# Kernel optimization log

Hardware: AMD Instinct MI355X
Metric: run time of the kernel (lower is better)

## Reference

```python
import jax, jax.numpy as jnp
import numpy as np
import math

B, SQ, SKV, H = 8, 1024, 1024, 1024
NH, HD = 16, 64  # num_attention_heads, attention_head_size


def setup_inputs() -> dict:
    key = jax.random.key(0)
    ks = jax.random.split(key, 6)
    s = 1.0 / math.sqrt(H)
    return {
        "hidden_states": jax.random.normal(ks[0], (B, SQ, H), jnp.float32),
        "keyvalue_states": jax.random.normal(ks[1], (B, SKV, H), jnp.float32),
        "attention_mask": jnp.zeros((B, 1, 1, SKV), jnp.float32),
        "Wq": jax.random.normal(ks[2], (H, H), jnp.float32) * s,
        "bq": jnp.zeros((H,), jnp.float32),
        "Wk": jax.random.normal(ks[3], (H, H), jnp.float32) * s,
        "bk": jnp.zeros((H,), jnp.float32),
        "Wv": jax.random.normal(ks[4], (H, H), jnp.float32) * s,
        "bv": jnp.zeros((H,), jnp.float32),
    }


def _split_heads(x):
    # [B, S, H] -> [B, NH, S, HD]
    b, s, _ = x.shape
    return x.reshape(b, s, NH, HD).transpose(0, 2, 1, 3)


def reference(hidden_states, keyvalue_states, attention_mask, Wq, bq, Wk, bk, Wv, bv):
    q = _split_heads(hidden_states @ Wq.T + bq)     # [B, NH, SQ, HD]
    k = _split_heads(keyvalue_states @ Wk.T + bk)   # [B, NH, SKV, HD]
    v = _split_heads(keyvalue_states @ Wv.T + bv)   # [B, NH, SKV, HD]
    scores = jnp.einsum("bhqd,bhkd->bhqk", q, k) / math.sqrt(HD)
    scores = scores + attention_mask                 # additive mask broadcast
    probs = jax.nn.softmax(scores, axis=-1)          # dropout = identity (eval)
    ctx = jnp.einsum("bhqk,bhkd->bhqd", probs, v)
    ctx = ctx.transpose(0, 2, 1, 3).reshape(hidden_states.shape[0], -1, NH * HD)
    return ctx
```

## Files before the change

### kernel.cpp

```cpp
#include <hip/hip_runtime.h>
#include <hip/hip_bf16.h>


typedef __attribute__((ext_vector_type(8))) short short8;
typedef __attribute__((ext_vector_type(4))) short short4v;
typedef __attribute__((ext_vector_type(4))) float f32x4;
typedef __attribute__((ext_vector_type(2))) float f32x2;
typedef __attribute__((ext_vector_type(16))) float f32x16;
typedef __attribute__((ext_vector_type(2))) unsigned uint2v;
typedef __attribute__((ext_vector_type(4))) int int4v;

#define AS1(p) ((const __attribute__((address_space(1))) void*)(p))
#define AS3(p) ((__attribute__((address_space(3))) void*)(p))

__device__ inline short f2bs(float x) {
    __hip_bfloat16 h = __float2bfloat16(x);
    return *reinterpret_cast<short*>(&h);
}

__global__ __launch_bounds__(256) void cvt_bf16(
    const float* __restrict__ s0, const float* __restrict__ s1,
    const float* __restrict__ s2, const float* __restrict__ s3,
    const float* __restrict__ s4,
    short* __restrict__ d0, short* __restrict__ d1,
    short* __restrict__ d2, short* __restrict__ d3, short* __restrict__ d4)
{
    const float* s; short* d; int n4;
    switch (blockIdx.y) {
        case 0: s = s0; d = d0; n4 = 2097152; break;
        case 1: s = s1; d = d1; n4 = 2097152; break;
        case 2: s = s2; d = d2; n4 = 262144;  break;
        case 3: s = s3; d = d3; n4 = 262144;  break;
        default: s = s4; d = d4; n4 = 262144; break;
    }
    for (int i = blockIdx.x * 256 + threadIdx.x; i < n4; i += gridDim.x * 256) {
        float4 v = ((const float4*)s)[i];
        short4v o;
        o.x = f2bs(v.x); o.y = f2bs(v.y); o.z = f2bs(v.z); o.w = f2bs(v.w);
        ((short4v*)d)[i] = o;
    }
}

__global__ __launch_bounds__(256, 2) void q_gemm(
    const short* __restrict__ hsb, const short* __restrict__ wqb,
    const float* __restrict__ bq, short* __restrict__ qo)
{
    __shared__ __align__(16) short As[128 * 64];
    __shared__ __align__(16) short Bs[128 * 64];

    const int t = threadIdx.x;
    const int lane = t & 63;
    const int wave = t >> 6;
    const int lane31 = lane & 31;
    const int hi = lane >> 5;
    const int wm = (wave & 1) * 64;
    const int wn = (wave >> 1) * 64;
    const int m0 = blockIdx.x * 128;
    const int n0 = blockIdx.y * 128;

    f32x16 acc[2][2] = {};

    for (int k0 = 0; k0 < 1024; k0 += 64) {
        #pragma unroll
        for (int i = 0; i < 4; ++i) {
            int c = i * 256 + t;
            int row = c >> 3;
            int gc = (c & 7) ^ (row & 7);
            __builtin_amdgcn_global_load_lds(
                AS1(&hsb[(size_t)(m0 + row) * 1024 + k0 + gc * 8]), AS3(&As[c * 8]), 16, 0, 0);
            __builtin_amdgcn_global_load_lds(
                AS1(&wqb[(size_t)(n0 + row) * 1024 + k0 + gc * 8]), AS3(&Bs[c * 8]), 16, 0, 0);
        }
        __syncthreads();

        #pragma unroll
        for (int kc = 0; kc < 4; ++kc) {
            short8 af[2], bf[2];
            #pragma unroll
            for (int mt = 0; mt < 2; ++mt) {
                int rr = wm + mt * 32 + lane31;
                af[mt] = *(short8*)&As[rr * 64 + ((kc * 2 + hi) ^ (rr & 7)) * 8];
            }
            #pragma unroll
            for (int nt = 0; nt < 2; ++nt) {
                int rn = wn + nt * 32 + lane31;
                bf[nt] = *(short8*)&Bs[rn * 64 + ((kc * 2 + hi) ^ (rn & 7)) * 8];
            }
            #pragma unroll
            for (int mt = 0; mt < 2; ++mt)
                #pragma unroll
                for (int nt = 0; nt < 2; ++nt)
                    acc[mt][nt] = __builtin_amdgcn_mfma_f32_32x32x16_bf16(
                        af[mt], bf[nt], acc[mt][nt], 0, 0, 0);
        }
        __syncthreads();
    }

    #pragma unroll
    for (int nt = 0; nt < 2; ++nt) {
        int col = n0 + wn + nt * 32 + lane31;
        float bb = bq[col];
        int h = col >> 6, d = col & 63;
        #pragma unroll
        for (int mt = 0; mt < 2; ++mt) {
            #pragma unroll
            for (int rg = 0; rg < 4; ++rg) {
                int m = m0 + wm + mt * 32 + rg * 8 + hi * 4;
                int b = m >> 10, s = m & 1023;
                size_t base = (size_t)((b * 16 + h) * 1024 + s) * 64 + d;
                #pragma unroll
                for (int r = 0; r < 4; ++r)
                    qo[base + (size_t)r * 64] = f2bs(acc[mt][nt][rg * 4 + r] + bb);
            }
        }
    }
}

__global__ __launch_bounds__(256, 2) void kv_gemm(
    const short* __restrict__ kvb,
    const short* __restrict__ wkb, const short* __restrict__ wvb,
    const float* __restrict__ bk, const float* __restrict__ bv,
    short* __restrict__ ko, short* __restrict__ vo)
{
    __shared__ __align__(16) short As[128 * 64];
    __shared__ __align__(16) short Bk[128 * 64];
    __shared__ __align__(16) short Bv[128 * 64];

    const int t = threadIdx.x;
    const int lane = t & 63;
    const int wave = t >> 6;
    const int lane31 = lane & 31;
    const int hi = lane >> 5;
    const int wm = (wave & 1) * 64;
    const int wn = (wave >> 1) * 64;
    const int m0 = blockIdx.x * 128;
    const int n0 = blockIdx.y * 128;

    f32x16 acck[2][2] = {};
    f32x16 accv[2][2] = {};

    for (int k0 = 0; k0 < 1024; k0 += 64) {
        #pragma unroll
        for (int i = 0; i < 4; ++i) {
            int c = i * 256 + t;
            int row = c >> 3;
            int gc = (c & 7) ^ (row & 7);
            __builtin_amdgcn_global_load_lds(
                AS1(&kvb[(size_t)(m0 + row) * 1024 + k0 + gc * 8]), AS3(&As[c * 8]), 16, 0, 0);
            __builtin_amdgcn_global_load_lds(
                AS1(&wkb[(size_t)(n0 + row) * 1024 + k0 + gc * 8]), AS3(&Bk[c * 8]), 16, 0, 0);
            __builtin_amdgcn_global_load_lds(
                AS1(&wvb[(size_t)(n0 + row) * 1024 + k0 + gc * 8]), AS3(&Bv[c * 8]), 16, 0, 0);
        }
        __syncthreads();

        #pragma unroll
        for (int kc = 0; kc < 4; ++kc) {
            short8 af[2], bfk[2], bfv[2];
            #pragma unroll
            for (int mt = 0; mt < 2; ++mt) {
                int rr = wm + mt * 32 + lane31;
                af[mt] = *(short8*)&As[rr * 64 + ((kc * 2 + hi) ^ (rr & 7)) * 8];
            }
            #pragma unroll
            for (int nt = 0; nt < 2; ++nt) {
                int rn = wn + nt * 32 + lane31;
                int off = rn * 64 + ((kc * 2 + hi) ^ (rn & 7)) * 8;
                bfk[nt] = *(short8*)&Bk[off];
                bfv[nt] = *(short8*)&Bv[off];
            }
            #pragma unroll
            for (int mt = 0; mt < 2; ++mt)
                #pragma unroll
                for (int nt = 0; nt < 2; ++nt) {
                    acck[mt][nt] = __builtin_amdgcn_mfma_f32_32x32x16_bf16(
                        af[mt], bfk[nt], acck[mt][nt], 0, 0, 0);
                    accv[mt][nt] = __builtin_amdgcn_mfma_f32_32x32x16_bf16(
                        af[mt], bfv[nt], accv[mt][nt], 0, 0, 0);
                }
        }
        __syncthreads();
    }

    #pragma unroll
    for (int nt = 0; nt < 2; ++nt) {
        int col = n0 + wn + nt * 32 + lane31;
        float bb = bk[col];
        int h = col >> 6, d = col & 63;
        #pragma unroll
        for (int mt = 0; mt < 2; ++mt) {
            #pragma unroll
            for (int rg = 0; rg < 4; ++rg) {
                int m = m0 + wm + mt * 32 + rg * 8 + hi * 4;
                int b = m >> 10, s = m & 1023;
                size_t base = (size_t)((b * 16 + h) * 1024 + s) * 64 + d;
                #pragma unroll
                for (int r = 0; r < 4; ++r)
                    ko[base + (size_t)r * 64] = f2bs(acck[mt][nt][rg * 4 + r] + bb);
            }
        }
    }
    #pragma unroll
    for (int nt = 0; nt < 2; ++nt) {
        int col = n0 + wn + nt * 32 + lane31;
        float bb = bv[col];
        int h = col >> 6, d = col & 63;
        #pragma unroll
        for (int mt = 0; mt < 2; ++mt) {
            #pragma unroll
            for (int rg = 0; rg < 4; ++rg) {
                int m = m0 + wm + mt * 32 + rg * 8 + hi * 4;
                int b = m >> 10, s = m & 1023;
                short4v pk;
                pk.x = f2bs(accv[mt][nt][rg * 4 + 0] + bb);
                pk.y = f2bs(accv[mt][nt][rg * 4 + 1] + bb);
                pk.z = f2bs(accv[mt][nt][rg * 4 + 2] + bb);
                pk.w = f2bs(accv[mt][nt][rg * 4 + 3] + bb);
                *(short4v*)&vo[(size_t)((b * 16 + h) * 64 + d) * 1024 + s] = pk;
            }
        }
    }
}

#define EXPC 0.18033688011112042f
#define LOG2E 1.4426950408889634f

__device__ inline uint2v half_swap(unsigned c, unsigned d, int hi) {
#if __has_builtin(__builtin_amdgcn_permlane32_swap)
    return __builtin_amdgcn_permlane32_swap(c, d, false, false);
#else
    unsigned send = hi ? c : d;
    unsigned recv = (unsigned)__shfl_xor((int)send, 32, 64);
    uint2v r;
    r.x = hi ? recv : c;
    r.y = hi ? d : recv;
    return r;
#endif
}

__device__ inline float fast_exp2(float x) {
#if __has_builtin(__builtin_amdgcn_exp2f)
    return __builtin_amdgcn_exp2f(x);
#else
    float r;
    asm("v_exp_f32 %0, %1" : "=v"(r) : "v"(x));
    return r;
#endif
}

__device__ inline unsigned cvt_pk_bf16(float a, float b) {
    unsigned r;
    asm("v_cvt_pk_bf16_f32 %0, %1, %2" : "=v"(r) : "v"(a), "v"(b));
    return r;
}

__global__ __launch_bounds__(256, 4) void attn(
    const short* __restrict__ q, const short* __restrict__ k,
    const short* __restrict__ vt, const float* __restrict__ mask,
    float* __restrict__ out)
{
    __shared__ __align__(16) short Ks[2][64 * 64];
    __shared__ __align__(16) short Vs[2][64 * 64];
    __shared__ __align__(16) float Ems[1024];

    const int t = threadIdx.x;
    const int lane = t & 63;
    const int wq = t >> 6;
    const int lane31 = lane & 31;
    const int hi = lane >> 5;

    const int id = blockIdx.x;
    const int bh = (id >> 6) * 8 + (id & 7);
    const int qt = (id >> 3) & 7;
    const int b = bh >> 4, h = bh & 15;

    const short* qbase = q + (size_t)(bh * 1024 + qt * 128) * 64;
    const short* kbase = k + (size_t)bh * 1024 * 64;
    const short* vbase = vt + (size_t)bh * 64 * 1024;

    {
        float4 mv = ((const float4*)(mask + b * 1024))[t];
        float4 o4;
        o4.x = mv.x * LOG2E; o4.y = mv.y * LOG2E;
        o4.z = mv.z * LOG2E; o4.w = mv.w * LOG2E;
        *(float4*)&Ems[t * 4] = o4;
    }

    short8 qf[4];
    #pragma unroll
    for (int kc = 0; kc < 4; ++kc)
        qf[kc] = *(const short8*)&qbase[(size_t)(wq * 32 + lane31) * 64 + kc * 16 + hi * 8];

    #pragma unroll
    for (int i = 0; i < 2; ++i) {
        int c = i * 256 + t;
        int row = c >> 3;
        int gc = (c & 7) ^ (row & 7);
        __builtin_amdgcn_global_load_lds(AS1(kbase + (size_t)row * 64 + gc * 8),
                                         AS3(&Ks[0][c * 8]), 16, 0, 0);
        __builtin_amdgcn_global_load_lds(AS1(vbase + (size_t)row * 1024 + gc * 8),
                                         AS3(&Vs[0][c * 8]), 16, 0, 0);
    }

    f32x16 o_acc[2] = {};
    f32x2 lacc = {0.f, 0.f};

    for (int kt = 0; kt < 16; ++kt) {
        __syncthreads();
        if (kt < 15) {
            int kv1 = (kt + 1) * 64;
            int nb = (kt + 1) & 1;
            #pragma unroll
            for (int i = 0; i < 2; ++i) {
                int c = i * 256 + t;
                int row = c >> 3;
                int gc = (c & 7) ^ (row & 7);
                __builtin_amdgcn_global_load_lds(
                    AS1(kbase + (size_t)(kv1 + row) * 64 + gc * 8),
                    AS3(&Ks[nb][c * 8]), 16, 0, 0);
                __builtin_amdgcn_global_load_lds(
                    AS1(vbase + (size_t)row * 1024 + kv1 + gc * 8),
                    AS3(&Vs[nb][c * 8]), 16, 0, 0);
            }
        }
        const short* ks_ = Ks[kt & 1];
        const short* vs_ = Vs[kt & 1];
        const int kv0 = kt * 64;

        f32x16 sacc[2] = {};
        #pragma unroll
        for (int kc = 0; kc < 4; ++kc) {
            #pragma unroll
            for (int mt = 0; mt < 2; ++mt) {
                int rr = mt * 32 + lane31;
                short8 ak = *(short8*)&ks_[rr * 64 + ((kc * 2 + hi) ^ (rr & 7)) * 8];
                sacc[mt] = __builtin_amdgcn_mfma_f32_32x32x16_bf16(ak, qf[kc], sacc[mt], 0, 0, 0);
            }
        }

        unsigned pk[2][4][2];
        #pragma unroll
        for (int mt = 0; mt < 2; ++mt) {
            #pragma unroll
            for (int rg = 0; rg < 4; ++rg) {
                int kvl = mt * 32 + rg * 8 + hi * 4;
                f32x4 mk = *(const f32x4*)&Ems[kv0 + kvl];
                f32x4 sv;
                sv.x = sacc[mt][rg * 4 + 0];
                sv.y = sacc[mt][rg * 4 + 1];
                sv.z = sacc[mt][rg * 4 + 2];
                sv.w = sacc[mt][rg * 4 + 3];
                f32x4 ev = sv * EXPC + mk;
                float p0 = fast_exp2(ev.x);
                float p1 = fast_exp2(ev.y);
                float p2 = fast_exp2(ev.z);
                float p3 = fast_exp2(ev.w);
                f32x2 pa; pa.x = p0; pa.y = p2;
                f32x2 pb; pb.x = p1; pb.y = p3;
                lacc += pa + pb;
                pk[mt][rg][0] = cvt_pk_bf16(p0, p1);
                pk[mt][rg][1] = cvt_pk_bf16(p2, p3);
            }
        }

        #pragma unroll
        for (int kc = 0; kc < 4; ++kc) {
            const int mt = kc >> 1, glo = (kc & 1) * 2;
            uint2v s0 = half_swap(pk[mt][glo][0], pk[mt][glo + 1][0], hi);
            uint2v s1 = half_swap(pk[mt][glo][1], pk[mt][glo + 1][1], hi);
            int4v fr; fr.x = (int)s0.x; fr.y = (int)s1.x; fr.z = (int)s0.y; fr.w = (int)s1.y;
            short8 ap = *(short8*)&fr;
            #pragma unroll
            for (int nt = 0; nt < 2; ++nt) {
                int rv = nt * 32 + lane31;
                short8 bv_ = *(short8*)&vs_[rv * 64 + ((kc * 2 + hi) ^ (rv & 7)) * 8];
                o_acc[nt] = __builtin_amdgcn_mfma_f32_32x32x16_bf16(ap, bv_, o_acc[nt], 0, 0, 0);
            }
        }
    }

    float l_sum = lacc.x + lacc.y;
    l_sum += __shfl_xor(l_sum, 32, 64);
    float invl = 1.f / l_sum;

    #pragma unroll
    for (int rg = 0; rg < 4; ++rg) {
        #pragma unroll
        for (int r = 0; r < 4; ++r) {
            int qrow_l = rg * 8 + hi * 4 + r;
            float lv = __shfl(invl, qrow_l, 64);
            int qrow = qt * 128 + wq * 32 + qrow_l;
            size_t base = (size_t)(b * 1024 + qrow) * 1024 + h * 64;
            #pragma unroll
            for (int nt = 0; nt < 2; ++nt)
                out[base + nt * 32 + lane31] = o_acc[nt][rg * 4 + r] * lv;
        }
    }
}

extern "C" void kernel_launch(void* const* d_in, const int* in_sizes, int n_in,
                              void* d_out, int out_size, void* d_ws, size_t ws_size,
                              hipStream_t stream) {
    const float* hs   = (const float*)d_in[0];
    const float* kvs  = (const float*)d_in[1];
    const float* mask = (const float*)d_in[2];
    const float* Wq   = (const float*)d_in[3];
    const float* bq   = (const float*)d_in[4];
    const float* Wk   = (const float*)d_in[5];
    const float* bk   = (const float*)d_in[6];
    const float* Wv   = (const float*)d_in[7];
    const float* bv   = (const float*)d_in[8];
    float* outp = (float*)d_out;

    const size_t big = (size_t)8 * 1024 * 1024;
    const size_t wsz = (size_t)1024 * 1024;
    short* q_ws  = (short*)d_ws;
    short* k_ws  = q_ws  + big;
    short* vt_ws = k_ws  + big;
    short* hsb   = vt_ws + big;
    short* kvb   = hsb   + big;
    short* wqb   = kvb   + big;
    short* wkb   = wqb   + wsz;
    short* wvb   = wkb   + wsz;

    cvt_bf16<<<dim3(1024, 5), 256, 0, stream>>>(hs, kvs, Wq, Wk, Wv,
                                                hsb, kvb, wqb, wkb, wvb);
    q_gemm<<<dim3(64, 8), 256, 0, stream>>>(hsb, wqb, bq, q_ws);
    kv_gemm<<<dim3(64, 8), 256, 0, stream>>>(kvb, wkb, wvb, bk, bv, k_ws, vt_ws);
    attn<<<dim3(1024), 256, 0, stream>>>(q_ws, k_ws, vt_ws, mask, outp);
}
```

Baseline: 230.4 us.

## Process two 32-row query tiles per wave to reuse K/V fragments

Each wave now handles 64 query rows instead of 32, so each block covers 256 query rows and the grid shrinks from 1024 to 512 blocks. Every K and V fragment read from LDS feeds two MFMAs, halving K/V LDS reads and global K/V tile loads per query row. Launch bounds drop to 2 blocks per SM to make room for the doubled accumulators and Q fragments, which lowers occupancy. With 512 blocks there are fewer waves to balance across CUs.

```diff
diff --git a/kernel.cpp b/kernel.cpp
--- a/kernel.cpp
+++ b/kernel.cpp
@@ -254,7 +254,7 @@
     return r;
 }
 
-__global__ __launch_bounds__(256, 4) void attn(
+__global__ __launch_bounds__(256, 2) void attn(
     const short* __restrict__ q, const short* __restrict__ k,
     const short* __restrict__ vt, const float* __restrict__ mask,
     float* __restrict__ out)
@@ -270,11 +270,11 @@
     const int hi = lane >> 5;
 
     const int id = blockIdx.x;
-    const int bh = (id >> 6) * 8 + (id & 7);
-    const int qt = (id >> 3) & 7;
+    const int bh = (id >> 5) * 8 + (id & 7);
+    const int qt = (id >> 3) & 3;
     const int b = bh >> 4, h = bh & 15;
 
-    const short* qbase = q + (size_t)(bh * 1024 + qt * 128) * 64;
+    const short* qbase = q + (size_t)(bh * 1024 + qt * 256) * 64;
     const short* kbase = k + (size_t)bh * 1024 * 64;
     const short* vbase = vt + (size_t)bh * 64 * 1024;
 
@@ -286,10 +286,13 @@
         *(float4*)&Ems[t * 4] = o4;
     }
 
-    short8 qf[4];
-    #pragma unroll
-    for (int kc = 0; kc < 4; ++kc)
-        qf[kc] = *(const short8*)&qbase[(size_t)(wq * 32 + lane31) * 64 + kc * 16 + hi * 8];
+    short8 qf[2][4];
+    #pragma unroll
+    for (int qh = 0; qh < 2; ++qh)
+        #pragma unroll
+        for (int kc = 0; kc < 4; ++kc)
+            qf[qh][kc] = *(const short8*)&qbase[
+                (size_t)(wq * 64 + qh * 32 + lane31) * 64 + kc * 16 + hi * 8];
 
     #pragma unroll
     for (int i = 0; i < 2; ++i) {
@@ -302,8 +305,8 @@
                                          AS3(&Vs[0][c * 8]), 16, 0, 0);
     }
 
-    f32x16 o_acc[2] = {};
-    f32x2 lacc = {0.f, 0.f};
+    f32x16 o_acc[2][2] = {};
+    f32x2 lacc[2] = {{0.f, 0.f}, {0.f, 0.f}};
 
     for (int kt = 0; kt < 16; ++kt) {
         __syncthreads();
@@ -327,73 +330,96 @@
         const short* vs_ = Vs[kt & 1];
         const int kv0 = kt * 64;
 
-        f32x16 sacc[2] = {};
+        f32x16 sacc[2][2] = {};
         #pragma unroll
         for (int kc = 0; kc < 4; ++kc) {
+            short8 ak[2];
             #pragma unroll
             for (int mt = 0; mt < 2; ++mt) {
                 int rr = mt * 32 + lane31;
-                short8 ak = *(short8*)&ks_[rr * 64 + ((kc * 2 + hi) ^ (rr & 7)) * 8];
-                sacc[mt] = __builtin_amdgcn_mfma_f32_32x32x16_bf16(ak, qf[kc], sacc[mt], 0, 0, 0);
-            }
-        }
-
-        unsigned pk[2][4][2];
+                ak[mt] = *(short8*)&ks_[rr * 64 + ((kc * 2 + hi) ^ (rr & 7)) * 8];
+            }
+            #pragma unroll
+            for (int qh = 0; qh < 2; ++qh)
+                #pragma unroll
+                for (int mt = 0; mt < 2; ++mt)
+                    sacc[qh][mt] = __builtin_amdgcn_mfma_f32_32x32x16_bf16(
+                        ak[mt], qf[qh][kc], sacc[qh][mt], 0, 0, 0);
+        }
+
+        unsigned pk[2][2][4][2];
         #pragma unroll
         for (int mt = 0; mt < 2; ++mt) {
             #pragma unroll
             for (int rg = 0; rg < 4; ++rg) {
                 int kvl = mt * 32 + rg * 8 + hi * 4;
                 f32x4 mk = *(const f32x4*)&Ems[kv0 + kvl];
-                f32x4 sv;
-                sv.x = sacc[mt][rg * 4 + 0];
-                sv.y = sacc[mt][rg * 4 + 1];
-                sv.z = sacc[mt][rg * 4 + 2];
-                sv.w = sacc[mt][rg * 4 + 3];
-                f32x4 ev = sv * EXPC + mk;
-                float p0 = fast_exp2(ev.x);
-                float p1 = fast_exp2(ev.y);
-                float p2 = fast_exp2(ev.z);
-                float p3 = fast_exp2(ev.w);
-                f32x2 pa; pa.x = p0; pa.y = p2;
-                f32x2 pb; pb.x = p1; pb.y = p3;
-                lacc += pa + pb;
-                pk[mt][rg][0] = cvt_pk_bf16(p0, p1);
-                pk[mt][rg][1] = cvt_pk_bf16(p2, p3);
+                #pragma unroll
+                for (int qh = 0; qh < 2; ++qh) {
+                    f32x4 sv;
+                    sv.x = sacc[qh][mt][rg * 4 + 0];
+                    sv.y = sacc[qh][mt][rg * 4 + 1];
+                    sv.z = sacc[qh][mt][rg * 4 + 2];
+                    sv.w = sacc[qh][mt][rg * 4 + 3];
+                    f32x4 ev = sv * EXPC + mk;
+                    float p0 = fast_exp2(ev.x);
+                    float p1 = fast_exp2(ev.y);
+                    float p2 = fast_exp2(ev.z);
+                    float p3 = fast_exp2(ev.w);
+                    f32x2 pa; pa.x = p0; pa.y = p2;
+                    f32x2 pb; pb.x = p1; pb.y = p3;
+                    lacc[qh] += pa + pb;
+                    pk[qh][mt][rg][0] = cvt_pk_bf16(p0, p1);
+                    pk[qh][mt][rg][1] = cvt_pk_bf16(p2, p3);
+                }
             }
         }
 
         #pragma unroll
         for (int kc = 0; kc < 4; ++kc) {
             const int mt = kc >> 1, glo = (kc & 1) * 2;
-            uint2v s0 = half_swap(pk[mt][glo][0], pk[mt][glo + 1][0], hi);
-            uint2v s1 = half_swap(pk[mt][glo][1], pk[mt][glo + 1][1], hi);
-            int4v fr; fr.x = (int)s0.x; fr.y = (int)s1.x; fr.z = (int)s0.y; fr.w = (int)s1.y;
-            short8 ap = *(short8*)&fr;
+            short8 bv_[2];
             #pragma unroll
             for (int nt = 0; nt < 2; ++nt) {
                 int rv = nt * 32 + lane31;
-                short8 bv_ = *(short8*)&vs_[rv * 64 + ((kc * 2 + hi) ^ (rv & 7)) * 8];
-                o_acc[nt] = __builtin_amdgcn_mfma_f32_32x32x16_bf16(ap, bv_, o_acc[nt], 0, 0, 0);
-            }
-        }
-    }
-
-    float l_sum = lacc.x + lacc.y;
-    l_sum += __shfl_xor(l_sum, 32, 64);
-    float invl = 1.f / l_sum;
-
-    #pragma unroll
-    for (int rg = 0; rg < 4; ++rg) {
-        #pragma unroll
-        for (int r = 0; r < 4; ++r) {
-            int qrow_l = rg * 8 + hi * 4 + r;
-            float lv = __shfl(invl, qrow_l, 64);
-            int qrow = qt * 128 + wq * 32 + qrow_l;
-            size_t base = (size_t)(b * 1024 + qrow) * 1024 + h * 64;
-            #pragma unroll
-            for (int nt = 0; nt < 2; ++nt)
-                out[base + nt * 32 + lane31] = o_acc[nt][rg * 4 + r] * lv;
+                bv_[nt] = *(short8*)&vs_[rv * 64 + ((kc * 2 + hi) ^ (rv & 7)) * 8];
+            }
+            #pragma unroll
+            for (int qh = 0; qh < 2; ++qh) {
+                uint2v s0 = half_swap(pk[qh][mt][glo][0], pk[qh][mt][glo + 1][0], hi);
+                uint2v s1 = half_swap(pk[qh][mt][glo][1], pk[qh][mt][glo + 1][1], hi);
+                int4v fr; fr.x = (int)s0.x; fr.y = (int)s1.x; fr.z = (int)s0.y; fr.w = (int)s1.y;
+                short8 ap = *(short8*)&fr;
+                #pragma unroll
+                for (int nt = 0; nt < 2; ++nt)
+                    o_acc[qh][nt] = __builtin_amdgcn_mfma_f32_32x32x16_bf16(
+                        ap, bv_[nt], o_acc[qh][nt], 0, 0, 0);
+            }
+        }
+    }
+
+    float invl[2];
+    #pragma unroll
+    for (int qh = 0; qh < 2; ++qh) {
+        float l_sum = lacc[qh].x + lacc[qh].y;
+        l_sum += __shfl_xor(l_sum, 32, 64);
+        invl[qh] = 1.f / l_sum;
+    }
+
+    #pragma unroll
+    for (int qh = 0; qh < 2; ++qh) {
+        #pragma unroll
+        for (int rg = 0; rg < 4; ++rg) {
+            #pragma unroll
+            for (int r = 0; r < 4; ++r) {
+                int qrow_l = rg * 8 + hi * 4 + r;
+                float lv = __shfl(invl[qh], qrow_l, 64);
+                int qrow = qt * 256 + wq * 64 + qh * 32 + qrow_l;
+                size_t base = (size_t)(b * 1024 + qrow) * 1024 + h * 64;
+                #pragma unroll
+                for (int nt = 0; nt < 2; ++nt)
+                    out[base + nt * 32 + lane31] = o_acc[qh][nt][rg * 4 + r] * lv;
+            }
         }
     }
 }
@@ -427,5 +453,5 @@
                                                 hsb, kvb, wqb, wkb, wvb);
     q_gemm<<<dim3(64, 8), 256, 0, stream>>>(hsb, wqb, bq, q_ws);
     kv_gemm<<<dim3(64, 8), 256, 0, stream>>>(kvb, wkb, wvb, bk, bv, k_ws, vt_ws);
-    attn<<<dim3(1024), 256, 0, stream>>>(q_ws, k_ws, vt_ws, mask, outp);
-}
+    attn<<<dim3(512), 256, 0, stream>>>(q_ws, k_ws, vt_ws, mask, outp);
+}
```

Result: no change. 227.7 us (-1.2%).

## Fuse activation bf16 conversion into projection GEMMs and prioritize attention MFMA phases

Applied to the files above, without the earlier changes.

The standalone conversion pass over hidden_states and keyvalue_states is removed. The Q and KV GEMMs now load fp32 activations through registers, convert them to packed bf16 and write them into swizzled LDS, so a full write and re-read of two 32MB activation tensors is avoided. Each GEMM block now reads fp32 activation tiles, which is twice the bytes per load, and these loads go through VGPRs instead of direct-to-LDS. The repeated reads of each tile across the eight N blocks also become fp32. Separately, the attention kernel raises wave priority around its MFMA sections with s_setprio.

```diff
diff --git a/kernel.cpp b/kernel.cpp
--- a/kernel.cpp
+++ b/kernel.cpp
@@ -18,31 +18,32 @@
     return *reinterpret_cast<short*>(&h);
 }
 
+__device__ inline unsigned cvt_pk_bf16(float a, float b) {
+    unsigned r;
+    asm("v_cvt_pk_bf16_f32 %0, %1, %2" : "=v"(r) : "v"(a), "v"(b));
+    return r;
+}
+
 __global__ __launch_bounds__(256) void cvt_bf16(
     const float* __restrict__ s0, const float* __restrict__ s1,
-    const float* __restrict__ s2, const float* __restrict__ s3,
-    const float* __restrict__ s4,
-    short* __restrict__ d0, short* __restrict__ d1,
-    short* __restrict__ d2, short* __restrict__ d3, short* __restrict__ d4)
+    const float* __restrict__ s2,
+    short* __restrict__ d0, short* __restrict__ d1, short* __restrict__ d2)
 {
-    const float* s; short* d; int n4;
+    const float* s; short* d;
     switch (blockIdx.y) {
-        case 0: s = s0; d = d0; n4 = 2097152; break;
-        case 1: s = s1; d = d1; n4 = 2097152; break;
-        case 2: s = s2; d = d2; n4 = 262144;  break;
-        case 3: s = s3; d = d3; n4 = 262144;  break;
-        default: s = s4; d = d4; n4 = 262144; break;
-    }
-    for (int i = blockIdx.x * 256 + threadIdx.x; i < n4; i += gridDim.x * 256) {
-        float4 v = ((const float4*)s)[i];
-        short4v o;
-        o.x = f2bs(v.x); o.y = f2bs(v.y); o.z = f2bs(v.z); o.w = f2bs(v.w);
-        ((short4v*)d)[i] = o;
-    }
+        case 0: s = s0; d = d0; break;
+        case 1: s = s1; d = d1; break;
+        default: s = s2; d = d2; break;
+    }
+    int i = blockIdx.x * 256 + threadIdx.x;
+    float4 v = ((const float4*)s)[i];
+    short4v o;
+    o.x = f2bs(v.x); o.y = f2bs(v.y); o.z = f2bs(v.z); o.w = f2bs(v.w);
+    ((short4v*)d)[i] = o;
 }
 
 __global__ __launch_bounds__(256, 2) void q_gemm(
-    const short* __restrict__ hsb, const short* __restrict__ wqb,
+    const float* __restrict__ hs, const short* __restrict__ wqb,
     const float* __restrict__ bq, short* __restrict__ qo)
 {
     __shared__ __align__(16) short As[128 * 64];
@@ -61,15 +62,27 @@
     f32x16 acc[2][2] = {};
 
     for (int k0 = 0; k0 < 1024; k0 += 64) {
+        float4 a0[4], a1[4];
         #pragma unroll
         for (int i = 0; i < 4; ++i) {
             int c = i * 256 + t;
             int row = c >> 3;
             int gc = (c & 7) ^ (row & 7);
             __builtin_amdgcn_global_load_lds(
-                AS1(&hsb[(size_t)(m0 + row) * 1024 + k0 + gc * 8]), AS3(&As[c * 8]), 16, 0, 0);
-            __builtin_amdgcn_global_load_lds(
                 AS1(&wqb[(size_t)(n0 + row) * 1024 + k0 + gc * 8]), AS3(&Bs[c * 8]), 16, 0, 0);
+            const float* src = &hs[(size_t)(m0 + row) * 1024 + k0 + gc * 8];
+            a0[i] = *(const float4*)src;
+            a1[i] = *(const float4*)(src + 4);
+        }
+        #pragma unroll
+        for (int i = 0; i < 4; ++i) {
+            int c = i * 256 + t;
+            int4v wv;
+            wv.x = (int)cvt_pk_bf16(a0[i].x, a0[i].y);
+            wv.y = (int)cvt_pk_bf16(a0[i].z, a0[i].w);
+            wv.z = (int)cvt_pk_bf16(a1[i].x, a1[i].y);
+            wv.w = (int)cvt_pk_bf16(a1[i].z, a1[i].w);
+            *(int4v*)&As[c * 8] = wv;
         }
         __syncthreads();
 
@@ -117,7 +130,7 @@
 }
 
 __global__ __launch_bounds__(256, 2) void kv_gemm(
-    const short* __restrict__ kvb,
+    const float* __restrict__ kvs,
     const short* __restrict__ wkb, const short* __restrict__ wvb,
     const float* __restrict__ bk, const float* __restrict__ bv,
     short* __restrict__ ko, short* __restrict__ vo)
@@ -140,17 +153,29 @@
     f32x16 accv[2][2] = {};
 
     for (int k0 = 0; k0 < 1024; k0 += 64) {
+        float4 a0[4], a1[4];
         #pragma unroll
         for (int i = 0; i < 4; ++i) {
             int c = i * 256 + t;
             int row = c >> 3;
             int gc = (c & 7) ^ (row & 7);
             __builtin_amdgcn_global_load_lds(
-                AS1(&kvb[(size_t)(m0 + row) * 1024 + k0 + gc * 8]), AS3(&As[c * 8]), 16, 0, 0);
-            __builtin_amdgcn_global_load_lds(
                 AS1(&wkb[(size_t)(n0 + row) * 1024 + k0 + gc * 8]), AS3(&Bk[c * 8]), 16, 0, 0);
             __builtin_amdgcn_global_load_lds(
                 AS1(&wvb[(size_t)(n0 + row) * 1024 + k0 + gc * 8]), AS3(&Bv[c * 8]), 16, 0, 0);
+            const float* src = &kvs[(size_t)(m0 + row) * 1024 + k0 + gc * 8];
+            a0[i] = *(const float4*)src;
+            a1[i] = *(const float4*)(src + 4);
+        }
+        #pragma unroll
+        for (int i = 0; i < 4; ++i) {
+            int c = i * 256 + t;
+            int4v wv;
+            wv.x = (int)cvt_pk_bf16(a0[i].x, a0[i].y);
+            wv.y = (int)cvt_pk_bf16(a0[i].z, a0[i].w);
+            wv.z = (int)cvt_pk_bf16(a1[i].x, a1[i].y);
+            wv.w = (int)cvt_pk_bf16(a1[i].z, a1[i].w);
+            *(int4v*)&As[c * 8] = wv;
         }
         __syncthreads();
 
@@ -248,12 +273,6 @@
 #endif
 }
 
-__device__ inline unsigned cvt_pk_bf16(float a, float b) {
-    unsigned r;
-    asm("v_cvt_pk_bf16_f32 %0, %1, %2" : "=v"(r) : "v"(a), "v"(b));
-    return r;
-}
-
 __global__ __launch_bounds__(256, 4) void attn(
     const short* __restrict__ q, const short* __restrict__ k,
     const short* __restrict__ vt, const float* __restrict__ mask,
@@ -328,6 +347,7 @@
         const int kv0 = kt * 64;
 
         f32x16 sacc[2] = {};
+        __builtin_amdgcn_s_setprio(1);
         #pragma unroll
         for (int kc = 0; kc < 4; ++kc) {
             #pragma unroll
@@ -337,6 +357,7 @@
                 sacc[mt] = __builtin_amdgcn_mfma_f32_32x32x16_bf16(ak, qf[kc], sacc[mt], 0, 0, 0);
             }
         }
+        __builtin_amdgcn_s_setprio(0);
 
         unsigned pk[2][4][2];
         #pragma unroll
@@ -363,6 +384,7 @@
             }
         }
 
+        __builtin_amdgcn_s_setprio(1);
         #pragma unroll
         for (int kc = 0; kc < 4; ++kc) {
             const int mt = kc >> 1, glo = (kc & 1) * 2;
@@ -377,6 +399,7 @@
                 o_acc[nt] = __builtin_amdgcn_mfma_f32_32x32x16_bf16(ap, bv_, o_acc[nt], 0, 0, 0);
             }
         }
+        __builtin_amdgcn_s_setprio(0);
     }
 
     float l_sum = lacc.x + lacc.y;
@@ -423,9 +446,8 @@
     short* wkb   = wqb   + wsz;
     short* wvb   = wkb   + wsz;
 
-    cvt_bf16<<<dim3(1024, 5), 256, 0, stream>>>(hs, kvs, Wq, Wk, Wv,
-                                                hsb, kvb, wqb, wkb, wvb);
-    q_gemm<<<dim3(64, 8), 256, 0, stream>>>(hsb, wqb, bq, q_ws);
-    kv_gemm<<<dim3(64, 8), 256, 0, stream>>>(kvb, wkb, wvb, bk, bv, k_ws, vt_ws);
+    cvt_bf16<<<dim3(1024, 3), 256, 0, stream>>>(Wq, Wk, Wv, wqb, wkb, wvb);
+    q_gemm<<<dim3(64, 8), 256, 0, stream>>>(hs, wqb, bq, q_ws);
+    kv_gemm<<<dim3(64, 8), 256, 0, stream>>>(kvs, wkb, wvb, bk, bv, k_ws, vt_ws);
     attn<<<dim3(1024), 256, 0, stream>>>(q_ws, k_ws, vt_ws, mask, outp);
 }
```

After: 244.3 us. 6.0% more time.
